# Performance work log

Measured on AMD Instinct MI355X. Metric: run time of the kernel, lower is better.

The kernel has to match this reference:

```python
import jax, jax.numpy as jnp
import numpy as np

NUM_HEADS = 16
HEAD_DIM = 64
SCALE = HEAD_DIM ** (-0.5)


def setup_inputs() -> dict:
    key = jax.random.key(0)
    ks = jax.random.split(key, 7)
    B, T, S, D = 8, 1024, 1500, 1024
    std = 1.0 / np.sqrt(D)
    return {
        "x": jax.random.normal(ks[0], (B, T, D), jnp.float32),
        "k": jax.random.normal(ks[1], (B, S, D), jnp.float32),
        "v": jax.random.normal(ks[2], (B, S, D), jnp.float32),
        "wq": jax.random.normal(ks[3], (D, D), jnp.float32) * std,
        "bq": jnp.zeros((D,), jnp.float32),
        "wo": jax.random.normal(ks[4], (D, D), jnp.float32) * std,
        "bo": jnp.zeros((D,), jnp.float32),
    }


def reference(x, k, v, wq, bq, wo, bo):
    B, T, D = x.shape
    H, Dh = NUM_HEADS, HEAD_DIM
    # q_proj (torch Linear: x @ W^T + b), pre-scaled
    q = (jnp.einsum("btd,ed->bte", x, wq) + bq) * SCALE
    q = q.reshape(B, T, H, Dh)                      # bthd
    kh = k.reshape(B, -1, H, Dh)                    # bshd
    vh = v.reshape(B, -1, H, Dh)
    scores = jnp.einsum("bthd,bshd->bhts", q, kh)   # full [B,H,T,S]
    probs = jax.nn.softmax(scores, axis=-1)
    out = jnp.einsum("bhts,bshd->bthd", probs, vh).reshape(B, T, D)
    return jnp.einsum("btd,ed->bte", out, wo) + bo
```

## Files before the change

### kernel.cpp

```cpp
#include <hip/hip_runtime.h>
#include <hip/hip_bf16.h>

typedef __attribute__((ext_vector_type(8))) short short8;
typedef __attribute__((ext_vector_type(4))) float floatx4;

#define B_ 8
#define T_ 1024
#define S_ 1500
#define SP 1536
#define D_ 1024
#define H_ 16
#define DH 64
#define SCALE2_ 0.1803368801111244f

__device__ __forceinline__ unsigned short f2bf(float f) {
  unsigned u = __float_as_uint(f);
  u += 0x7fffu + ((u >> 16) & 1u);
  return (unsigned short)(u >> 16);
}

__device__ __forceinline__ floatx4 mfma16(short8 a, short8 b, floatx4 c) {
  return __builtin_amdgcn_mfma_f32_16x16x32_bf16(a, b, c, 0, 0, 0);
}

#define N1C (B_ * T_ * D_ / 4)
#define N2C (D_ * D_ / 4)
__global__ void cast3_kernel(const float* __restrict__ x, const float* __restrict__ wq,
                             const float* __restrict__ wo, unsigned short* __restrict__ xb,
                             unsigned short* __restrict__ wqb,
                             unsigned short* __restrict__ wob) {
  int i = blockIdx.x * blockDim.x + threadIdx.x;
  const float* src;
  unsigned short* dst;
  int j;
  if (i < N1C) {
    src = x; dst = xb; j = i;
  } else if (i < N1C + N2C) {
    src = wq; dst = wqb; j = i - N1C;
  } else {
    src = wo; dst = wob; j = i - N1C - N2C;
  }
  float4 v = ((const float4*)src)[j];
  ushort4 o;
  o.x = f2bf(v.x); o.y = f2bf(v.y); o.z = f2bf(v.z); o.w = f2bf(v.w);
  ((ushort4*)dst)[j] = o;
}

__global__ void pack_k_kernel(const float* __restrict__ k,
                              unsigned short* __restrict__ kb) {
  int i = blockIdx.x * blockDim.x + threadIdx.x;
  int dh4 = (i & 15) * 4;
  int j = i >> 4;
  int s = j % SP;
  int bh = j / SP;
  if (bh >= B_ * H_) return;
  int b = bh >> 4, h = bh & 15;
  int p = s & 31;
  int src = (s & ~31) + ((p >> 2) & 3) * 8 + ((p >> 4) & 1) * 4 + (p & 3);
  ushort4 o;
  if (src < S_) {
    float4 v = *(const float4*)(k + (((size_t)(b * S_ + src) * H_ + h) * DH) + dh4);
    o.x = f2bf(v.x); o.y = f2bf(v.y); o.z = f2bf(v.z); o.w = f2bf(v.w);
  } else {
    o = make_ushort4(0, 0, 0, 0);
  }
  *(ushort4*)(kb + ((size_t)bh * SP + s) * DH + dh4) = o;
}

__global__ void pack_vt_kernel(const float* __restrict__ v,
                               unsigned short* __restrict__ vt) {
  __shared__ unsigned short tile[64][72];
  int st = blockIdx.x, bh = blockIdx.y;
  int b = bh >> 4, h = bh & 15;
  int s0 = st * 64;
  int t = threadIdx.x;
  for (int i = t; i < 1024; i += 256) {
    int sl = i >> 4, dh4 = (i & 15) * 4;
    float4 val = make_float4(0.f, 0.f, 0.f, 0.f);
    if (s0 + sl < S_)
      val = *(const float4*)(v + ((size_t)((b * S_ + s0 + sl) * H_ + h)) * DH + dh4);
    tile[dh4 + 0][sl] = f2bf(val.x);
    tile[dh4 + 1][sl] = f2bf(val.y);
    tile[dh4 + 2][sl] = f2bf(val.z);
    tile[dh4 + 3][sl] = f2bf(val.w);
  }
  __syncthreads();
  for (int i = t; i < 1024; i += 256) {
    int d = i >> 4, s4 = (i & 15) * 4;
    ushort4 o;
    o.x = tile[d][s4]; o.y = tile[d][s4 + 1]; o.z = tile[d][s4 + 2]; o.w = tile[d][s4 + 3];
    *(ushort4*)(vt + ((size_t)bh * DH + d) * SP + s0 + s4) = o;
  }
}

#define BK 32
#define ASTR 40
__global__ __launch_bounds__(256) void gemm_bt(const unsigned short* __restrict__ A,
                                               const unsigned short* __restrict__ Bm,
                                               const float* __restrict__ bias,
                                               void* __restrict__ outp, int epi) {
  __shared__ unsigned short As[128 * ASTR];
  __shared__ unsigned short Bs[128 * ASTR];
  const int K = 1024;
  int t = threadIdx.x;
  int m0 = blockIdx.y * 128, n0 = blockIdx.x * 128;
  int w = t >> 6, lane = t & 63, quad = lane >> 4, l16 = lane & 15;
  int mw = (w & 1) * 64, nw = (w >> 1) * 64;
  int lrow = t >> 2, lcol = (t & 3) * 8;

  const unsigned short* Ag = A + (size_t)(m0 + lrow) * K + lcol;
  const unsigned short* Bg = Bm + (size_t)(n0 + lrow) * K + lcol;

  floatx4 acc[4][4];
#pragma unroll
  for (int i = 0; i < 4; i++)
#pragma unroll
    for (int j = 0; j < 4; j++) {
      floatx4 z = {0.f, 0.f, 0.f, 0.f};
      acc[i][j] = z;
    }

  int4 a0 = *(const int4*)(Ag);
  int4 a1 = *(const int4*)(Ag + (size_t)64 * K);
  int4 b0 = *(const int4*)(Bg);
  int4 b1 = *(const int4*)(Bg + (size_t)64 * K);

  for (int kt = 0; kt < K / BK; kt++) {
    __syncthreads();
    *(int4*)&As[lrow * ASTR + lcol] = a0;
    *(int4*)&As[(lrow + 64) * ASTR + lcol] = a1;
    *(int4*)&Bs[lrow * ASTR + lcol] = b0;
    *(int4*)&Bs[(lrow + 64) * ASTR + lcol] = b1;
    __syncthreads();
    if (kt + 1 < K / BK) {
      a0 = *(const int4*)(Ag + (kt + 1) * BK);
      a1 = *(const int4*)(Ag + (size_t)64 * K + (kt + 1) * BK);
      b0 = *(const int4*)(Bg + (kt + 1) * BK);
      b1 = *(const int4*)(Bg + (size_t)64 * K + (kt + 1) * BK);
    }
    short8 af[4], bf[4];
#pragma unroll
    for (int mi = 0; mi < 4; mi++)
      af[mi] = *(const short8*)&As[(mw + mi * 16 + l16) * ASTR + quad * 8];
#pragma unroll
    for (int ni = 0; ni < 4; ni++)
      bf[ni] = *(const short8*)&Bs[(nw + ni * 16 + l16) * ASTR + quad * 8];
#pragma unroll
    for (int mi = 0; mi < 4; mi++)
#pragma unroll
      for (int ni = 0; ni < 4; ni++)
        acc[mi][ni] = mfma16(af[mi], bf[ni], acc[mi][ni]);
  }

#pragma unroll
  for (int mi = 0; mi < 4; mi++)
#pragma unroll
    for (int ni = 0; ni < 4; ni++) {
      int row = m0 + mw + mi * 16 + quad * 4;
      int col = n0 + nw + ni * 16 + l16;
      float bcol = bias[col];
#pragma unroll
      for (int r = 0; r < 4; r++) {
        float val = acc[mi][ni][r] + bcol;
        int rr = row + r;
        if (epi == 0) {
          int b = rr >> 10, tt = rr & 1023, h = col >> 6, dh = col & 63;
          ((unsigned short*)outp)[(((size_t)(b * 16 + h) * 1024) + tt) * 64 + dh] =
              f2bf(val * SCALE2_);
        } else {
          ((float*)outp)[(size_t)rr * 1024 + col] = val;
        }
      }
    }
}

__global__ __launch_bounds__(512, 4) void attn_kernel(
    const unsigned short* __restrict__ qs, const unsigned short* __restrict__ kb,
    const unsigned short* __restrict__ vt, unsigned short* __restrict__ ob) {
  __shared__ unsigned short Ks[128 * 72];
  __shared__ unsigned short Vs[64 * 136];
  int ttile = blockIdx.x, bh = blockIdx.y;
  int b = bh >> 4, h = bh & 15;
  int t = threadIdx.x, w = t >> 6, lane = t & 63, quad = lane >> 4, l16 = lane & 15;

  const unsigned short* qp =
      qs + ((size_t)bh * T_ + ttile * 128 + w * 16 + l16) * DH + quad * 8;
  short8 qa0 = *(const short8*)(qp);
  short8 qa1 = *(const short8*)(qp + 32);

  const unsigned short* kbase = kb + (size_t)bh * SP * DH;
  const unsigned short* vbase = vt + (size_t)bh * DH * SP;

  floatx4 o[4];
#pragma unroll
  for (int i = 0; i < 4; i++) {
    floatx4 z = {0.f, 0.f, 0.f, 0.f};
    o[i] = z;
  }
  float mrow = -1e30f, lrow = 0.f;

  for (int s0 = 0; s0 < SP; s0 += 128) {
    __syncthreads();
    {
      const int4* src = (const int4*)(kbase + (size_t)s0 * DH);
#pragma unroll
      for (int i = t; i < 128 * DH / 8; i += 512) {
        int row = i >> 3, c = i & 7;
        *(int4*)&Ks[row * 72 + c * 8] = src[i];
      }
#pragma unroll
      for (int i = t; i < 64 * 128 / 8; i += 512) {
        int d = i >> 4, c = i & 15;
        *(int4*)&Vs[d * 136 + c * 8] = *(const int4*)(vbase + (size_t)d * SP + s0 + c * 8);
      }
    }
    __syncthreads();

    floatx4 sc[8];
#pragma unroll
    for (int nb = 0; nb < 8; nb++) {
      short8 k0 = *(const short8*)&Ks[(nb * 16 + l16) * 72 + quad * 8];
      short8 k1 = *(const short8*)&Ks[(nb * 16 + l16) * 72 + 32 + quad * 8];
      floatx4 a = {0.f, 0.f, 0.f, 0.f};
      a = mfma16(k0, qa0, a);
      a = mfma16(k1, qa1, a);
      sc[nb] = a;
    }
    if (s0 + 128 > S_) {
#pragma unroll
      for (int nb = 0; nb < 8; nb++)
#pragma unroll
        for (int r = 0; r < 4; r++) {
          int s_act = s0 + (nb >> 1) * 32 + quad * 8 + (nb & 1) * 4 + r;
          if (s_act >= S_) sc[nb][r] = -1e30f;
        }
    }

    float mx = -1e30f;
#pragma unroll
    for (int nb = 0; nb < 8; nb++) {
      float a0m = fmaxf(sc[nb][0], sc[nb][1]);
      float a1m = fmaxf(sc[nb][2], sc[nb][3]);
      mx = fmaxf(mx, fmaxf(a0m, a1m));
    }
    mx = fmaxf(mx, __shfl_xor(mx, 16));
    mx = fmaxf(mx, __shfl_xor(mx, 32));
    float mnew = fmaxf(mrow, mx);
    float alpha = exp2f(mrow - mnew);
    mrow = mnew;
    float rs = 0.f;
#pragma unroll
    for (int nb = 0; nb < 8; nb++) {
#pragma unroll
      for (int r = 0; r < 4; r++) {
        float p = exp2f(sc[nb][r] - mnew);
        sc[nb][r] = p;
        rs += p;
      }
    }
    rs += __shfl_xor(rs, 16);
    rs += __shfl_xor(rs, 32);
    lrow = lrow * alpha + rs;
#pragma unroll
    for (int db = 0; db < 4; db++) {
      o[db][0] *= alpha; o[db][1] *= alpha; o[db][2] *= alpha; o[db][3] *= alpha;
    }

#pragma unroll
    for (int c = 0; c < 4; c++) {
      union { short8 v; __hip_bfloat162 h[4]; } pk;
      pk.h[0] = __float22bfloat162_rn(make_float2(sc[2 * c][0], sc[2 * c][1]));
      pk.h[1] = __float22bfloat162_rn(make_float2(sc[2 * c][2], sc[2 * c][3]));
      pk.h[2] = __float22bfloat162_rn(make_float2(sc[2 * c + 1][0], sc[2 * c + 1][1]));
      pk.h[3] = __float22bfloat162_rn(make_float2(sc[2 * c + 1][2], sc[2 * c + 1][3]));
#pragma unroll
      for (int db = 0; db < 4; db++) {
        short8 vf = *(const short8*)&Vs[(db * 16 + l16) * 136 + c * 32 + quad * 8];
        o[db] = mfma16(vf, pk.v, o[db]);
      }
    }
  }

  float inv = 1.0f / lrow;
  int tg = ttile * 128 + w * 16 + l16;
#pragma unroll
  for (int db = 0; db < 4; db++) {
    int dh = db * 16 + quad * 4;
    union { ushort4 s4; __hip_bfloat162 h[2]; } st;
    st.h[0] = __float22bfloat162_rn(make_float2(o[db][0] * inv, o[db][1] * inv));
    st.h[1] = __float22bfloat162_rn(make_float2(o[db][2] * inv, o[db][3] * inv));
    *(ushort4*)(ob + ((size_t)(b * T_ + tg) * H_ + h) * DH + dh) = st.s4;
  }
}

extern "C" void kernel_launch(void* const* d_in, const int* in_sizes, int n_in,
                              void* d_out, int out_size, void* d_ws, size_t ws_size,
                              hipStream_t stream) {
  const float* x  = (const float*)d_in[0];
  const float* k  = (const float*)d_in[1];
  const float* v  = (const float*)d_in[2];
  const float* wq = (const float*)d_in[3];
  const float* bq = (const float*)d_in[4];
  const float* wo = (const float*)d_in[5];
  const float* bo = (const float*)d_in[6];
  float* out = (float*)d_out;

  char* ws = (char*)d_ws;
  unsigned short* xb  = (unsigned short*)(ws + 0);
  unsigned short* wqb = (unsigned short*)(ws + 16777216);
  unsigned short* wob = (unsigned short*)(ws + 18874368);
  unsigned short* kbp = (unsigned short*)(ws + 20971520);
  unsigned short* vtp = (unsigned short*)(ws + 46137344);
  unsigned short* qsp = (unsigned short*)(ws + 71303168);
  unsigned short* obp = (unsigned short*)(ws + 88080384);

  {
    int blocks = (N1C + 2 * N2C) / 256;
    cast3_kernel<<<blocks, 256, 0, stream>>>(x, wq, wo, xb, wqb, wob);
  }
  {
    int groups = B_ * H_ * SP * 16;
    pack_k_kernel<<<groups / 256, 256, 0, stream>>>(k, kbp);
    pack_vt_kernel<<<dim3(SP / 64, B_ * H_), 256, 0, stream>>>(v, vtp);
  }
  gemm_bt<<<dim3(D_ / 128, B_ * T_ / 128), 256, 0, stream>>>(xb, wqb, bq, qsp, 0);
  attn_kernel<<<dim3(T_ / 128, B_ * H_), 512, 0, stream>>>(qsp, kbp, vtp, obp);
  gemm_bt<<<dim3(D_ / 128, B_ * T_ / 128), 256, 0, stream>>>(obp, wob, bo, out, 1);
}
```

Before: 361.2 us.

## Use direct global-to-LDS loads with XOR-swizzled layout in projection GEMM

Replaces the register-staged global loads plus LDS stores in the projection GEMM with global_load_lds direct-to-LDS transfers. The padded LDS layout becomes an unpadded one with an XOR swizzle to avoid bank conflicts, and launch bounds request 4 blocks per SM. This removes register staging and VGPR pressure, but it also drops the software prefetch, so each k-step now waits on its own load with no overlap.

```diff
diff --git a/kernel.cpp b/kernel.cpp
--- a/kernel.cpp
+++ b/kernel.cpp
@@ -21,6 +21,12 @@
 
 __device__ __forceinline__ floatx4 mfma16(short8 a, short8 b, floatx4 c) {
   return __builtin_amdgcn_mfma_f32_16x16x32_bf16(a, b, c, 0, 0, 0);
+}
+
+__device__ __forceinline__ void gload_lds16(const unsigned short* g, unsigned short* l) {
+  __builtin_amdgcn_global_load_lds(
+      (const __attribute__((address_space(1))) unsigned int*)g,
+      (__attribute__((address_space(3))) unsigned int*)(unsigned long)(uintptr_t)l, 16, 0, 0);
 }
 
 #define N1C (B_ * T_ * D_ / 4)
@@ -94,22 +100,28 @@
 }
 
 #define BK 32
-#define ASTR 40
-__global__ __launch_bounds__(256) void gemm_bt(const unsigned short* __restrict__ A,
-                                               const unsigned short* __restrict__ Bm,
-                                               const float* __restrict__ bias,
-                                               void* __restrict__ outp, int epi) {
-  __shared__ unsigned short As[128 * ASTR];
-  __shared__ unsigned short Bs[128 * ASTR];
+__global__ __launch_bounds__(256, 4) void gemm_bt(const unsigned short* __restrict__ A,
+                                                  const unsigned short* __restrict__ Bm,
+                                                  const float* __restrict__ bias,
+                                                  void* __restrict__ outp, int epi) {
+  __shared__ unsigned short As[128 * BK];
+  __shared__ unsigned short Bs[128 * BK];
   const int K = 1024;
   int t = threadIdx.x;
   int m0 = blockIdx.y * 128, n0 = blockIdx.x * 128;
   int w = t >> 6, lane = t & 63, quad = lane >> 4, l16 = lane & 15;
   int mw = (w & 1) * 64, nw = (w >> 1) * 64;
-  int lrow = t >> 2, lcol = (t & 3) * 8;
-
-  const unsigned short* Ag = A + (size_t)(m0 + lrow) * K + lcol;
-  const unsigned short* Bg = Bm + (size_t)(n0 + lrow) * K + lcol;
+
+  int rloc = lane >> 2, c = lane & 3;
+  int g = c ^ (((w * 16 + rloc) >> 1) & 3);
+  const unsigned short* pa0 = A + (size_t)(m0 + w * 16 + rloc) * K + g * 8;
+  const unsigned short* pa1 = pa0 + (size_t)64 * K;
+  const unsigned short* pb0 = Bm + (size_t)(n0 + w * 16 + rloc) * K + g * 8;
+  const unsigned short* pb1 = pb0 + (size_t)64 * K;
+  unsigned short* lA0 = &As[(w * 16) * BK];
+  unsigned short* lA1 = &As[(64 + w * 16) * BK];
+  unsigned short* lB0 = &Bs[(w * 16) * BK];
+  unsigned short* lB1 = &Bs[(64 + w * 16) * BK];
 
   floatx4 acc[4][4];
 #pragma unroll
@@ -120,31 +132,30 @@
       acc[i][j] = z;
     }
 
-  int4 a0 = *(const int4*)(Ag);
-  int4 a1 = *(const int4*)(Ag + (size_t)64 * K);
-  int4 b0 = *(const int4*)(Bg);
-  int4 b1 = *(const int4*)(Bg + (size_t)64 * K);
+  int arow = mw + l16;
+  int brow = nw + l16;
 
   for (int kt = 0; kt < K / BK; kt++) {
     __syncthreads();
-    *(int4*)&As[lrow * ASTR + lcol] = a0;
-    *(int4*)&As[(lrow + 64) * ASTR + lcol] = a1;
-    *(int4*)&Bs[lrow * ASTR + lcol] = b0;
-    *(int4*)&Bs[(lrow + 64) * ASTR + lcol] = b1;
+    gload_lds16(pa0 + kt * BK, lA0);
+    gload_lds16(pa1 + kt * BK, lA1);
+    gload_lds16(pb0 + kt * BK, lB0);
+    gload_lds16(pb1 + kt * BK, lB1);
     __syncthreads();
-    if (kt + 1 < K / BK) {
-      a0 = *(const int4*)(Ag + (kt + 1) * BK);
-      a1 = *(const int4*)(Ag + (size_t)64 * K + (kt + 1) * BK);
-      b0 = *(const int4*)(Bg + (kt + 1) * BK);
-      b1 = *(const int4*)(Bg + (size_t)64 * K + (kt + 1) * BK);
-    }
+
     short8 af[4], bf[4];
 #pragma unroll
-    for (int mi = 0; mi < 4; mi++)
-      af[mi] = *(const short8*)&As[(mw + mi * 16 + l16) * ASTR + quad * 8];
-#pragma unroll
-    for (int ni = 0; ni < 4; ni++)
-      bf[ni] = *(const short8*)&Bs[(nw + ni * 16 + l16) * ASTR + quad * 8];
+    for (int mi = 0; mi < 4; mi++) {
+      int r = arow + mi * 16;
+      int pc = quad ^ ((r >> 1) & 3);
+      af[mi] = *(const short8*)&As[r * BK + pc * 8];
+    }
+#pragma unroll
+    for (int ni = 0; ni < 4; ni++) {
+      int r = brow + ni * 16;
+      int pc = quad ^ ((r >> 1) & 3);
+      bf[ni] = *(const short8*)&Bs[r * BK + pc * 8];
+    }
 #pragma unroll
     for (int mi = 0; mi < 4; mi++)
 #pragma unroll
```

Measured after the change: 346.8 us. 4.0% less time.
